# Kernel tuning notes

Measured on AMD Instinct MI355X. Metric: run time of the kernel, lower is better.

Reference implementation:

```python
import jax, jax.numpy as jnp
import numpy as np

B, T = 128, 51            # batch, token sequence length (cond token prepended -> T+1=52)
C, H = 1024, 16           # embed_dim, n_head
L = 8                     # total Blocks: 4 in trans_base + 4 in trans_head
F = 4 * C                 # fc_rate * embed_dim
V = 1024                  # num_vq
CLIP = 512
EPS = 1e-5


def sincos_pe(seq_len, dim):
    # faithful to pos_encoding.PE1d_sincos
    pos = np.arange(seq_len, dtype=np.float32)[:, None]
    div = np.exp(np.arange(0, dim, 2, dtype=np.float32) * (-np.log(10000.0) / dim))
    pe = np.zeros((seq_len, dim), np.float32)
    pe[:, 0::2] = np.sin(pos * div)
    pe[:, 1::2] = np.cos(pos * div)
    return jnp.asarray(pe)


def setup_inputs() -> dict:
    key = jax.random.key(0)
    ks = jax.random.split(key, 12)
    s = 0.02  # init std per _init_weights
    nrm = lambda k, shape: jax.random.normal(k, shape, jnp.float32) * s
    return dict(
        idx=jax.random.randint(ks[0], (B, T), 0, V + 2),
        clip_feature=jax.random.normal(ks[1], (B, CLIP), jnp.float32),
        tok_emb=nrm(ks[2], (V + 2, C)),
        cond_w=nrm(ks[3], (CLIP, C)), cond_b=jnp.zeros((C,), jnp.float32),
        ln1_w=jnp.ones((L, C), jnp.float32), ln1_b=jnp.zeros((L, C), jnp.float32),
        wq=nrm(ks[4], (L, C, C)), bq=jnp.zeros((L, C), jnp.float32),
        wk=nrm(ks[5], (L, C, C)), bk=jnp.zeros((L, C), jnp.float32),
        wv=nrm(ks[6], (L, C, C)), bv=jnp.zeros((L, C), jnp.float32),
        wp=nrm(ks[7], (L, C, C)), bp=jnp.zeros((L, C), jnp.float32),
        ln2_w=jnp.ones((L, C), jnp.float32), ln2_b=jnp.zeros((L, C), jnp.float32),
        w1=nrm(ks[8], (L, C, F)), b1=jnp.zeros((L, F), jnp.float32),
        w2=nrm(ks[9], (L, F, C)), b2=jnp.zeros((L, C), jnp.float32),
        lnf_w=jnp.ones((C,), jnp.float32), lnf_b=jnp.zeros((C,), jnp.float32),
        head_w=nrm(ks[10], (C, V + 1)),
    )


def _ln(x, w, b):
    m = jnp.mean(x, axis=-1, keepdims=True)
    v = jnp.var(x, axis=-1, keepdims=True)
    return (x - m) * jax.lax.rsqrt(v + EPS) * w + b


def _block(x, ln1w, ln1b, wq, bq, wk, bk, wv, bv, wp, bp, ln2w, ln2b, w1, b1, w2, b2):
    b_, t_, c_ = x.shape
    d = c_ // H
    h = _ln(x, ln1w, ln1b)
    q = (h @ wq + bq).reshape(b_, t_, H, d).transpose(0, 2, 1, 3)  # [B,H,T,d]
    k = (h @ wk + bk).reshape(b_, t_, H, d).transpose(0, 2, 1, 3)
    v = (h @ wv + bv).reshape(b_, t_, H, d).transpose(0, 2, 1, 3)
    att = jnp.einsum('bhqd,bhkd->bhqk', q, k) * (1.0 / np.sqrt(d))
    causal = jnp.tril(jnp.ones((t_, t_), bool))
    att = jnp.where(causal, att, -jnp.inf)
    att = jax.nn.softmax(att, axis=-1)
    y = jnp.einsum('bhqk,bhkd->bhqd', att, v).transpose(0, 2, 1, 3).reshape(b_, t_, c_)
    x = x + y @ wp + bp
    h2 = _ln(x, ln2w, ln2b)
    x = x + jax.nn.gelu(h2 @ w1 + b1, approximate=False) @ w2 + b2
    return x


def reference(idx, clip_feature, tok_emb, cond_w, cond_b,
              ln1_w, ln1_b, wq, bq, wk, bk, wv, bv, wp, bp,
              ln2_w, ln2_b, w1, b1, w2, b2, lnf_w, lnf_b, head_w):
    # CrossCondTransBase: cond token + token embeddings + sinusoidal pos embed
    cond = (clip_feature @ cond_w + cond_b)[:, None, :]           # [B,1,C]
    tok = tok_emb[idx]                                            # [B,T,C]
    x = jnp.concatenate([cond, tok], axis=1)                      # [B,T+1,C]
    x = x + sincos_pe(x.shape[1], C)[None, :, :]
    # 4 base blocks + 4 head blocks (identical structure, stacked params)
    for i in range(L):
        x = _block(x, ln1_w[i], ln1_b[i], wq[i], bq[i], wk[i], bk[i],
                   wv[i], bv[i], wp[i], bp[i], ln2_w[i], ln2_b[i],
                   w1[i], b1[i], w2[i], b2[i])
    x = _ln(x, lnf_w, lnf_b)
    logits = x @ head_w                                           # [B,T+1,num_vq+1]
    return logits
```

## Files before the change

### kernel.cpp

```cpp
#include <hip/hip_runtime.h>

using bf16x8 = __attribute__((ext_vector_type(8))) __bf16;
using short8 = __attribute__((ext_vector_type(8))) short;
using u16x8  = __attribute__((ext_vector_type(8))) unsigned short;
using u16x4  = __attribute__((ext_vector_type(4))) unsigned short;
using f32x4  = __attribute__((ext_vector_type(4))) float;

#define DEVI __device__ __forceinline__

DEVI unsigned short f2bf(float f) {
  union { float f; unsigned u; } un; un.f = f;
  unsigned r = un.u + 0x7fffu + ((un.u >> 16) & 1u);
  return (unsigned short)(r >> 16);
}

typedef const __attribute__((address_space(1))) void* gas1_t;
typedef __attribute__((address_space(3))) void* las3_t;

DEVI void gload16(const void* g, void* lds) {
  __builtin_amdgcn_global_load_lds(
      reinterpret_cast<gas1_t>(reinterpret_cast<unsigned long long>(g)),
      reinterpret_cast<las3_t>(static_cast<unsigned>(reinterpret_cast<unsigned long long>(lds))),
      16, 0, 0);
}

#define VMW(n) asm volatile("s_waitcnt vmcnt(" #n ")" ::: "memory")
#define LGK0   do { asm volatile("s_waitcnt lgkmcnt(0)" ::: "memory"); __builtin_amdgcn_sched_barrier(0); } while (0)
#define BARS   do { __builtin_amdgcn_s_barrier(); __builtin_amdgcn_sched_barrier(0); } while (0)

__global__ void __launch_bounds__(256)
transpose_cvt(const float* __restrict__ src, unsigned short* __restrict__ dst,
              int K, int N, int Nrows, long srcStride, long dstStride) {
  src += (size_t)blockIdx.z * srcStride;
  dst += (size_t)blockIdx.z * dstStride;
  __shared__ float tile[32][33];
  const int n0 = blockIdx.x * 32, k0 = blockIdx.y * 32;
  const int tx = threadIdx.x & 31, ty = threadIdx.x >> 5;
#pragma unroll
  for (int i = 0; i < 4; ++i) {
    const int kk = ty + i * 8;
    const int n = n0 + tx;
    tile[kk][tx] = (n < N) ? src[(size_t)(k0 + kk) * N + n] : 0.f;
  }
  __syncthreads();
#pragma unroll
  for (int i = 0; i < 4; ++i) {
    const int nn = ty + i * 8;
    const int n = n0 + nn;
    if (n < Nrows) dst[(size_t)n * K + k0 + tx] = f2bf(tile[tx][nn]);
  }
}

__global__ void __launch_bounds__(256)
concat_bias(const float* __restrict__ bq, const float* __restrict__ bk,
            const float* __restrict__ bv, float* __restrict__ ob) {
  const int i = blockIdx.x * 256 + threadIdx.x;
  if (i >= 8 * 3072) return;
  const int l = i / 3072, c = i - l * 3072;
  float v;
  if (c < 1024)      v = bq[l * 1024 + c];
  else if (c < 2048) v = bk[l * 1024 + c - 1024];
  else               v = bv[l * 1024 + c - 2048];
  ob[i] = v;
}

__global__ void __launch_bounds__(256)
embed_kernel(const int* __restrict__ idx, const float* __restrict__ clip,
             const float* __restrict__ tok_emb, const float* __restrict__ cond_w,
             const float* __restrict__ cond_b, float* __restrict__ x) {
  const int row = blockIdx.x;
  const int b = row / 52, t = row - b * 52;
  const int c0 = threadIdx.x * 4;
  float e[4];
  if (t == 0) {
    e[0] = cond_b[c0]; e[1] = cond_b[c0 + 1]; e[2] = cond_b[c0 + 2]; e[3] = cond_b[c0 + 3];
    for (int k = 0; k < 512; ++k) {
      const float cf = clip[b * 512 + k];
      const float4 wv = *(const float4*)&cond_w[k * 1024 + c0];
      e[0] += cf * wv.x; e[1] += cf * wv.y; e[2] += cf * wv.z; e[3] += cf * wv.w;
    }
  } else {
    const int tok = idx[b * 51 + t - 1];
    const float4 tv = *(const float4*)&tok_emb[(size_t)tok * 1024 + c0];
    e[0] = tv.x; e[1] = tv.y; e[2] = tv.z; e[3] = tv.w;
  }
  const float nl = -9.2103403719761836f / 1024.0f;
#pragma unroll
  for (int j = 0; j < 4; ++j) {
    const int c = c0 + j;
    const float dv = expf((float)(c & ~1) * nl);
    const float ang = (float)t * dv;
    e[j] += (c & 1) ? cosf(ang) : sinf(ang);
  }
  float4 o; o.x = e[0]; o.y = e[1]; o.z = e[2]; o.w = e[3];
  *(float4*)&x[(size_t)row * 1024 + c0] = o;
}

__global__ void __launch_bounds__(256)
ln_kernel(const float* __restrict__ x, const float* __restrict__ w,
          const float* __restrict__ bsh, unsigned short* __restrict__ out) {
  const size_t row = blockIdx.x;
  const int tid = threadIdx.x;
  const float4 v = *(const float4*)&x[row * 1024 + tid * 4];
  float s1 = v.x + v.y + v.z + v.w;
  float s2 = v.x * v.x + v.y * v.y + v.z * v.z + v.w * v.w;
#pragma unroll
  for (int m = 1; m < 64; m <<= 1) { s1 += __shfl_xor(s1, m); s2 += __shfl_xor(s2, m); }
  __shared__ float red[8];
  const int wid = tid >> 6;
  if ((tid & 63) == 0) { red[wid] = s1; red[4 + wid] = s2; }
  __syncthreads();
  s1 = red[0] + red[1] + red[2] + red[3];
  s2 = red[4] + red[5] + red[6] + red[7];
  const float mean = s1 * (1.0f / 1024.0f);
  const float var  = s2 * (1.0f / 1024.0f) - mean * mean;
  const float rstd = rsqrtf(var + 1e-5f);
  const float4 wv = *(const float4*)&w[tid * 4];
  const float4 bv = *(const float4*)&bsh[tid * 4];
  ushort4 o;
  o.x = f2bf((v.x - mean) * rstd * wv.x + bv.x);
  o.y = f2bf((v.y - mean) * rstd * wv.y + bv.y);
  o.z = f2bf((v.z - mean) * rstd * wv.z + bv.z);
  o.w = f2bf((v.w - mean) * rstd * wv.w + bv.w);
  *(ushort4*)&out[row * 1024 + tid * 4] = o;
}

__global__ void __launch_bounds__(256)
ln_sum_kernel(const float* __restrict__ xold, const float* __restrict__ part,
              long pstride, int S, const float* __restrict__ fcb,
              const float* __restrict__ w, const float* __restrict__ bsh,
              float* __restrict__ xnew, unsigned short* __restrict__ hout) {
  const size_t row = blockIdx.x;
  const int tid = threadIdx.x;
  const float4 xv = *(const float4*)&xold[row * 1024 + tid * 4];
  const float4 bb = *(const float4*)&fcb[tid * 4];
  float e0 = xv.x + bb.x, e1 = xv.y + bb.y, e2 = xv.z + bb.z, e3 = xv.w + bb.w;
  for (int s = 0; s < S; ++s) {
    const float4 p = *(const float4*)&part[(size_t)s * pstride + row * 1024 + tid * 4];
    e0 += p.x; e1 += p.y; e2 += p.z; e3 += p.w;
  }
  float s1 = e0 + e1 + e2 + e3;
  float s2 = e0 * e0 + e1 * e1 + e2 * e2 + e3 * e3;
#pragma unroll
  for (int m = 1; m < 64; m <<= 1) { s1 += __shfl_xor(s1, m); s2 += __shfl_xor(s2, m); }
  __shared__ float red[8];
  const int wid = tid >> 6;
  if ((tid & 63) == 0) { red[wid] = s1; red[4 + wid] = s2; }
  __syncthreads();
  s1 = red[0] + red[1] + red[2] + red[3];
  s2 = red[4] + red[5] + red[6] + red[7];
  const float mean = s1 * (1.0f / 1024.0f);
  const float var  = s2 * (1.0f / 1024.0f) - mean * mean;
  const float rstd = rsqrtf(var + 1e-5f);
  float4 xo; xo.x = e0; xo.y = e1; xo.z = e2; xo.w = e3;
  *(float4*)&xnew[row * 1024 + tid * 4] = xo;
  const float4 wv = *(const float4*)&w[tid * 4];
  const float4 bv = *(const float4*)&bsh[tid * 4];
  ushort4 o;
  o.x = f2bf((e0 - mean) * rstd * wv.x + bv.x);
  o.y = f2bf((e1 - mean) * rstd * wv.y + bv.y);
  o.z = f2bf((e2 - mean) * rstd * wv.z + bv.z);
  o.w = f2bf((e3 - mean) * rstd * wv.w + bv.w);
  *(ushort4*)&hout[row * 1024 + tid * 4] = o;
}

template <int EPI>
__global__ void __launch_bounds__(512, 2)
gemm256(const unsigned short* __restrict__ A, const unsigned short* __restrict__ WT,
        const float* __restrict__ bias, void* outp,
        int Kfull, int N, int k_len, int ny, int nz) {
  constexpr bool SWAP = (EPI == 0 || EPI == 1);
  __shared__ unsigned short smem[49152];
  const int tid = threadIdx.x;
  const int lane = tid & 63;
  const int wid = tid >> 6;
  const int lrow = lane & 15, lkg = lane >> 4;
  const int wm = wid >> 2, wn = wid & 3;

  const int nwg = gridDim.x;
  int bid = blockIdx.x;
  {
    const int q = nwg >> 3, r = nwg & 7;
    const int xcd = bid & 7, i = bid >> 3;
    bid = ((xcd < r) ? xcd * (q + 1) : r * (q + 1) + (xcd - r) * q) + i;
  }
  const int nxy = nwg / nz;
  const int z = bid / nxy;
  const int rem = bid - z * nxy;
  const int nx = nxy / ny;
  const int yt = rem / nx;
  const int xt = rem - yt * nx;
  const long m0 = (long)xt * 256;
  const long n0 = (long)yt * 256;
  const int kb = z * k_len;

  const unsigned short* ag[2];
  const unsigned short* bg[2];
#pragma unroll
  for (int j = 0; j < 2; ++j) {
    const int c = tid + j * 512;
    const int f = c >> 6, kg = (c >> 4) & 3, r = c & 15;
    ag[j] = A  + (m0 + f * 16 + r) * (long)Kfull + kb + kg * 8;
    bg[j] = WT + (n0 + f * 16 + r) * (long)Kfull + kb + kg * 8;
  }
  const int lo0 = wid * 512;
  const int lo1 = 4096 + wid * 512;

  f32x4 acc[8][4] = {};
  const int T = k_len >> 5;

  auto STAGE = [&](int t) {
    const int bo = (t % 3) * 16384;
    const long kt = (long)t * 32;
    gload16(ag[0] + kt, smem + bo + lo0);
    gload16(ag[1] + kt, smem + bo + lo1);
    gload16(bg[0] + kt, smem + bo + 8192 + lo0);
    gload16(bg[1] + kt, smem + bo + 8192 + lo1);
  };

  STAGE(0); STAGE(1);

  for (int t = 0; t < T; ++t) {
    if (t + 1 < T) VMW(4);
    else           VMW(0);
    BARS;
    if (t + 2 < T) STAGE(t + 2);
    const int bo = (t % 3) * 16384;
    bf16x8 afr[8], bfr[4];
#pragma unroll
    for (int m = 0; m < 8; ++m) afr[m] = *(const bf16x8*)&smem[bo + (wm * 8 + m) * 512 + lane * 8];
#pragma unroll
    for (int n = 0; n < 4; ++n) bfr[n] = *(const bf16x8*)&smem[bo + 8192 + (wn * 4 + n) * 512 + lane * 8];
    LGK0;
    __builtin_amdgcn_s_setprio(1);
#pragma unroll
    for (int m = 0; m < 8; ++m)
#pragma unroll
      for (int n = 0; n < 4; ++n) {
        if constexpr (SWAP)
          acc[m][n] = __builtin_amdgcn_mfma_f32_16x16x32_bf16(bfr[n], afr[m], acc[m][n], 0, 0, 0);
        else
          acc[m][n] = __builtin_amdgcn_mfma_f32_16x16x32_bf16(afr[m], bfr[n], acc[m][n], 0, 0, 0);
      }
    __builtin_amdgcn_s_setprio(0);
  }

  if constexpr (SWAP) {
#pragma unroll
    for (int p = 0; p < 2; ++p) {
      __syncthreads();
      if (wm == p) {
#pragma unroll
        for (int m = 0; m < 8; ++m) {
          const int rowl = m * 16 + lrow;
          const unsigned rb = (unsigned)rowl * 512;
          const unsigned sw = (unsigned)(rowl & 7) << 4;
#pragma unroll
          for (int n = 0; n < 4; ++n) {
            const int colb = wn * 64 + n * 16 + lkg * 4;
            const float4 bv = *(const float4*)&bias[n0 + colb];
            float v0 = acc[m][n][0] + bv.x;
            float v1 = acc[m][n][1] + bv.y;
            float v2 = acc[m][n][2] + bv.z;
            float v3 = acc[m][n][3] + bv.w;
            if constexpr (EPI == 1) {
              v0 = 0.5f * v0 * (1.0f + erff(v0 * 0.70710678118654752f));
              v1 = 0.5f * v1 * (1.0f + erff(v1 * 0.70710678118654752f));
              v2 = 0.5f * v2 * (1.0f + erff(v2 * 0.70710678118654752f));
              v3 = 0.5f * v3 * (1.0f + erff(v3 * 0.70710678118654752f));
            }
            u16x4 o = { f2bf(v0), f2bf(v1), f2bf(v2), f2bf(v3) };
            *(u16x4*)((char*)smem + ((rb + colb * 2) ^ sw)) = o;
          }
        }
      }
      __syncthreads();
      unsigned short* out = (unsigned short*)outp;
#pragma unroll
      for (int i = 0; i < 8; ++i) {
        const int idx = tid + i * 512;
        const int rowl = idx >> 5, c32 = idx & 31;
        const unsigned byteoff = ((unsigned)rowl * 512 + (unsigned)c32 * 16) ^ ((unsigned)(rowl & 7) << 4);
        const u16x8 v = *(const u16x8*)((const char*)smem + byteoff);
        *(u16x8*)&out[(m0 + p * 128 + rowl) * (long)N + n0 + c32 * 8] = v;
      }
    }
  } else {
    float* out = (float*)outp + (size_t)z * ((size_t)(nxy / ny) * 256) * N;
#pragma unroll
    for (int n = 0; n < 4; ++n) {
      const int col = (int)n0 + wn * 64 + n * 16 + lrow;
#pragma unroll
      for (int m = 0; m < 8; ++m) {
        const long rowb = m0 + wm * 128 + m * 16 + lkg * 4;
#pragma unroll
        for (int r = 0; r < 4; ++r)
          out[(rowb + r) * (long)N + col] = acc[m][n][r];
      }
    }
  }
}

template <int EPI>
__global__ void __launch_bounds__(256)
gemm128(const unsigned short* __restrict__ A, const unsigned short* __restrict__ WT,
        const float* __restrict__ bias, const float* res, void* outp,
        int Kfull, int N, int k_len, int ny, int nz) {
  __shared__ unsigned short smem[24576];
  const int tid = threadIdx.x;
  const int lane = tid & 63;
  const int wid = tid >> 6;
  const int lrow = lane & 15, lkg = lane >> 4;
  const int wr = wid >> 1, wc = wid & 1;

  const int nwg = gridDim.x;
  int bid = blockIdx.x;
  {
    const int q = nwg >> 3, r = nwg & 7;
    const int xcd = bid & 7, i = bid >> 3;
    bid = ((xcd < r) ? xcd * (q + 1) : r * (q + 1) + (xcd - r) * q) + i;
  }
  const int nxy = nwg / nz;
  const int z = bid / nxy;
  const int rem = bid - z * nxy;
  const int nx = nxy / ny;
  const int yt = rem / nx;
  const int xt = rem - yt * nx;
  const long m0 = (long)xt * 128;
  const long n0 = (long)yt * 128;
  const int kb = z * k_len;

  const unsigned short* a0 = A + (m0 + (wid * 2 + 0) * 16 + lrow) * (long)Kfull + kb + lkg * 8;
  const unsigned short* a1 = A + (m0 + (wid * 2 + 1) * 16 + lrow) * (long)Kfull + kb + lkg * 8;
  const unsigned short* b0 = WT + (n0 + (wid * 2 + 0) * 16 + lrow) * (long)Kfull + kb + lkg * 8;
  const unsigned short* b1 = WT + (n0 + (wid * 2 + 1) * 16 + lrow) * (long)Kfull + kb + lkg * 8;
  const int so0 = (wid * 2 + 0) * 512, so1 = (wid * 2 + 1) * 512;

  f32x4 acc[4][4] = {};
  const int T = k_len >> 5;

  auto STAGE = [&](int t) {
    const int boff = (t % 3) * 8192;
    const int kt = t * 32;
    gload16(a0 + kt, smem + boff + so0);
    gload16(a1 + kt, smem + boff + so1);
    gload16(b0 + kt, smem + boff + 4096 + so0);
    gload16(b1 + kt, smem + boff + 4096 + so1);
  };

  STAGE(0);
  STAGE(1);

  for (int t = 0; t < T; ++t) {
    if (t + 1 < T) asm volatile("s_waitcnt vmcnt(4)" ::: "memory");
    else           asm volatile("s_waitcnt vmcnt(0)" ::: "memory");
    __builtin_amdgcn_s_barrier();
    __builtin_amdgcn_sched_barrier(0);
    if (t + 2 < T) STAGE(t + 2);
    const int cb = (t % 3) * 8192;
    bf16x8 af[4], bf8[4];
#pragma unroll
    for (int m = 0; m < 4; ++m) af[m] = *(const bf16x8*)&smem[cb + (wr * 4 + m) * 512 + lane * 8];
#pragma unroll
    for (int n = 0; n < 4; ++n) bf8[n] = *(const bf16x8*)&smem[cb + 4096 + (wc * 4 + n) * 512 + lane * 8];
#pragma unroll
    for (int m = 0; m < 4; ++m)
#pragma unroll
      for (int n = 0; n < 4; ++n)
        acc[m][n] = __builtin_amdgcn_mfma_f32_16x16x32_bf16(af[m], bf8[n], acc[m][n], 0, 0, 0);
  }
  __syncthreads();

#pragma unroll
  for (int n = 0; n < 4; ++n) {
    const int col = (int)n0 + wc * 64 + n * 16 + lrow;
    const bool cv = col < N;
    float bv = 0.f;
    if (EPI == 2) bv = cv ? bias[col] : 0.f;
#pragma unroll
    for (int m = 0; m < 4; ++m) {
      const long rowb = m0 + wr * 64 + m * 16 + lkg * 4;
#pragma unroll
      for (int r = 0; r < 4; ++r) {
        float v = acc[m][n][r] + bv;
        if (cv) {
          if constexpr (EPI == 2)
            ((float*)outp)[(rowb + r) * (long)N + col] = res[(rowb + r) * (long)N + col] + v;
          else
            ((float*)outp)[(rowb + r) * (long)N + col] = v;
        }
      }
    }
  }
}

__global__ void __launch_bounds__(256)
attn_kernel(const unsigned short* __restrict__ qkv,
            unsigned short* __restrict__ attno) {
  __shared__ unsigned short qA[4096];
  __shared__ unsigned short kB[4096];
  __shared__ unsigned short vB[4096];
  __shared__ unsigned short pA[4096];
  const int bh = blockIdx.x;
  const int b = bh >> 4, h = bh & 15;
  const int tid = threadIdx.x;
  const int lane = tid & 63;
  const int wid = tid >> 6;
  const int lrow = lane & 15, lkg = lane >> 4;

  for (int i = tid; i < 512; i += 256) {
    const int row = i >> 3;
    const int dc = i & 7;
    short8 qv = {}, kv = {}, vv = {};
    if (row < 52) {
      const unsigned short* base = qkv + ((size_t)(b * 52 + row)) * 3072 + h * 64 + dc * 8;
      qv = *(const short8*)(base);
      kv = *(const short8*)(base + 1024);
      vv = *(const short8*)(base + 2048);
    }
    *(short8*)&qA[(row >> 4) * 1024 + dc * 128 + (row & 15) * 8] = qv;
    *(short8*)&kB[(row >> 4) * 1024 + dc * 128 + (row & 15) * 8] = kv;
#pragma unroll
    for (int j = 0; j < 8; ++j) {
      const int d = dc * 8 + j;
      vB[(d >> 4) * 1024 + (row >> 3) * 128 + (d & 15) * 8 + (row & 7)] = (unsigned short)vv[j];
    }
  }
  __syncthreads();

  f32x4 sacc[4] = {};
#pragma unroll
  for (int s = 0; s < 2; ++s) {
    const bf16x8 a = *(const bf16x8*)&qA[wid * 1024 + s * 512 + lane * 8];
#pragma unroll
    for (int c = 0; c < 4; ++c) {
      const bf16x8 bb = *(const bf16x8*)&kB[c * 1024 + s * 512 + lane * 8];
      sacc[c] = __builtin_amdgcn_mfma_f32_16x16x32_bf16(a, bb, sacc[c], 0, 0, 0);
    }
  }

#pragma unroll
  for (int r = 0; r < 4; ++r) {
    const int trow = wid * 16 + lkg * 4 + r;
    float sv[4];
#pragma unroll
    for (int c = 0; c < 4; ++c) {
      const int kp = c * 16 + lrow;
      sv[c] = (kp <= trow && kp < 52) ? sacc[c][r] * 0.125f : -3.0e38f;
    }
    float mx = fmaxf(fmaxf(sv[0], sv[1]), fmaxf(sv[2], sv[3]));
#pragma unroll
    for (int m = 1; m < 16; m <<= 1) mx = fmaxf(mx, __shfl_xor(mx, m));
    float p[4], sum = 0.f;
#pragma unroll
    for (int c = 0; c < 4; ++c) { p[c] = __expf(sv[c] - mx); sum += p[c]; }
#pragma unroll
    for (int m = 1; m < 16; m <<= 1) sum += __shfl_xor(sum, m);
    const float inv = 1.0f / sum;
#pragma unroll
    for (int c = 0; c < 4; ++c) {
      const int kp = c * 16 + lrow;
      pA[wid * 1024 + (kp >> 3) * 128 + (lkg * 4 + r) * 8 + (kp & 7)] = f2bf(p[c] * inv);
    }
  }
  __syncthreads();

  f32x4 oacc[4] = {};
#pragma unroll
  for (int s = 0; s < 2; ++s) {
    const bf16x8 a = *(const bf16x8*)&pA[wid * 1024 + s * 512 + lane * 8];
#pragma unroll
    for (int db = 0; db < 4; ++db) {
      const bf16x8 bb = *(const bf16x8*)&vB[db * 1024 + s * 512 + lane * 8];
      oacc[db] = __builtin_amdgcn_mfma_f32_16x16x32_bf16(a, bb, oacc[db], 0, 0, 0);
    }
  }
#pragma unroll
  for (int db = 0; db < 4; ++db)
#pragma unroll
    for (int r = 0; r < 4; ++r) {
      const int trow = wid * 16 + lkg * 4 + r;
      if (trow < 52) {
        const int d = db * 16 + lrow;
        attno[((size_t)(b * 52 + trow)) * 1024 + h * 64 + d] = f2bf(oacc[db][r]);
      }
    }
}

extern "C" void kernel_launch(void* const* d_in, const int* in_sizes, int n_in,
                              void* d_out, int out_size, void* d_ws, size_t ws_size,
                              hipStream_t stream) {
  const int*   idx    = (const int*)d_in[0];
  const float* clip   = (const float*)d_in[1];
  const float* tok    = (const float*)d_in[2];
  const float* cond_w = (const float*)d_in[3];
  const float* cond_b = (const float*)d_in[4];
  const float* ln1w   = (const float*)d_in[5];
  const float* ln1b   = (const float*)d_in[6];
  const float* wq     = (const float*)d_in[7];
  const float* bq     = (const float*)d_in[8];
  const float* wk     = (const float*)d_in[9];
  const float* bk     = (const float*)d_in[10];
  const float* wv     = (const float*)d_in[11];
  const float* bv     = (const float*)d_in[12];
  const float* wp     = (const float*)d_in[13];
  const float* bp     = (const float*)d_in[14];
  const float* ln2w   = (const float*)d_in[15];
  const float* ln2b   = (const float*)d_in[16];
  const float* w1     = (const float*)d_in[17];
  const float* b1     = (const float*)d_in[18];
  const float* w2     = (const float*)d_in[19];
  const float* b2     = (const float*)d_in[20];
  const float* lnfw   = (const float*)d_in[21];
  const float* lnfb   = (const float*)d_in[22];
  const float* headw  = (const float*)d_in[23];

  const int M = 6656;
  char* ws = (char*)d_ws;
  size_t off = 0;
  auto alloc = [&](size_t bytes) -> void* {
    void* p = ws + off;
    off += (bytes + 255) & ~(size_t)255;
    return p;
  };

  unsigned short* qkvT  = (unsigned short*)alloc((size_t)8 * 3072 * 1024 * 2);
  unsigned short* wpT   = (unsigned short*)alloc((size_t)8 * 1024 * 1024 * 2);
  unsigned short* w1T   = (unsigned short*)alloc((size_t)8 * 4096 * 1024 * 2);
  unsigned short* w2T   = (unsigned short*)alloc((size_t)8 * 1024 * 4096 * 2);
  unsigned short* headT = (unsigned short*)alloc((size_t)1152 * 1024 * 2);
  float*          qkvB  = (float*)alloc((size_t)8 * 3072 * 4);
  float*          xbuf  = (float*)alloc((size_t)M * 1024 * 4);
  unsigned short* hbuf  = (unsigned short*)alloc((size_t)M * 1024 * 2);
  unsigned short* big   = (unsigned short*)alloc((size_t)M * 4096 * 2);
  unsigned short* attno = (unsigned short*)alloc((size_t)M * 1024 * 2);
  float*          pbuf  = (float*)alloc((size_t)2 * M * 1024 * 4);
  unsigned short* qkv  = big;
  unsigned short* mlph = big;
  const long ps1024 = (long)M * 1024;

  const dim3 tb(256);
  const dim3 tb512(512);
  transpose_cvt<<<dim3(32, 32, 8), tb, 0, stream>>>(wq, qkvT,                        1024, 1024, 1024, (long)1024 * 1024, (long)3072 * 1024);
  transpose_cvt<<<dim3(32, 32, 8), tb, 0, stream>>>(wk, qkvT + (size_t)1024 * 1024,  1024, 1024, 1024, (long)1024 * 1024, (long)3072 * 1024);
  transpose_cvt<<<dim3(32, 32, 8), tb, 0, stream>>>(wv, qkvT + (size_t)2048 * 1024,  1024, 1024, 1024, (long)1024 * 1024, (long)3072 * 1024);
  transpose_cvt<<<dim3(32, 32, 8), tb, 0, stream>>>(wp, wpT,  1024, 1024, 1024, (long)1024 * 1024, (long)1024 * 1024);
  transpose_cvt<<<dim3(128, 32, 8), tb, 0, stream>>>(w1, w1T, 1024, 4096, 4096, (long)1024 * 4096, (long)4096 * 1024);
  transpose_cvt<<<dim3(32, 128, 8), tb, 0, stream>>>(w2, w2T, 4096, 1024, 1024, (long)4096 * 1024, (long)1024 * 4096);
  transpose_cvt<<<dim3(36, 32, 1), tb, 0, stream>>>(headw, headT, 1024, 1025, 1152, 0, 0);
  concat_bias<<<dim3(96), tb, 0, stream>>>(bq, bk, bv, qkvB);
  embed_kernel<<<dim3(M), tb, 0, stream>>>(idx, clip, tok, cond_w, cond_b, xbuf);
  ln_kernel<<<dim3(M), tb, 0, stream>>>(xbuf, ln1w, ln1b, hbuf);

  for (int l = 0; l < 8; ++l) {
    gemm256<0><<<dim3(312), tb512, 0, stream>>>(hbuf, qkvT + (size_t)l * 3072 * 1024,
                                                qkvB + l * 3072, qkv, 1024, 3072, 1024, 12, 1);
    attn_kernel<<<dim3(2048), tb, 0, stream>>>(qkv, attno);
    gemm128<2><<<dim3(52 * 8), tb, 0, stream>>>(attno, wpT + (size_t)l * 1024 * 1024,
                                                bp + l * 1024, xbuf, xbuf, 1024, 1024, 1024, 8, 1);
    ln_kernel<<<dim3(M), tb, 0, stream>>>(xbuf, ln2w + l * 1024, ln2b + l * 1024, hbuf);
    gemm256<1><<<dim3(416), tb512, 0, stream>>>(hbuf, w1T + (size_t)l * 4096 * 1024,
                                                b1 + l * 4096, mlph, 1024, 4096, 1024, 16, 1);
    gemm256<4><<<dim3(208), tb512, 0, stream>>>(mlph, w2T + (size_t)l * 1024 * 4096,
                                                nullptr, pbuf, 4096, 1024, 2048, 4, 2);
    if (l < 7)
      ln_sum_kernel<<<dim3(M), tb, 0, stream>>>(xbuf, pbuf, ps1024, 2, b2 + l * 1024,
                                                ln1w + (l + 1) * 1024, ln1b + (l + 1) * 1024, xbuf, hbuf);
    else
      ln_sum_kernel<<<dim3(M), tb, 0, stream>>>(xbuf, pbuf, ps1024, 2, b2 + l * 1024,
                                                lnfw, lnfb, xbuf, hbuf);
  }
  gemm128<3><<<dim3(52 * 9), tb, 0, stream>>>(hbuf, headT, nullptr, nullptr, d_out, 1024, 1025, 1024, 9, 1);
}
```

Before: 3.305 ms.

## Switch 256-tile GEMM to double-buffered 64-wide K stages with single-pass epilogue

The 256x256 GEMM now stages 64 K-elements per step into two 64KB-total LDS buffers instead of three 32-wide buffers, issuing loads in two 32-wide halves interleaved with compute. The epilogue writes the whole 256x256 bf16 tile to LDS in one pass rather than two halves, removing two barriers. Block-to-tile mapping in both GEMM kernels is changed to iterate N tiles fastest, altering L2 reuse patterns. The larger LDS footprint (128KB) may reduce occupancy below the two blocks per CU the launch bounds request.

```diff
diff --git a/kernel.cpp b/kernel.cpp
--- a/kernel.cpp
+++ b/kernel.cpp
@@ -170,7 +170,7 @@
         const float* __restrict__ bias, void* outp,
         int Kfull, int N, int k_len, int ny, int nz) {
   constexpr bool SWAP = (EPI == 0 || EPI == 1);
-  __shared__ unsigned short smem[49152];
+  __shared__ unsigned short smem[65536];
   const int tid = threadIdx.x;
   const int lane = tid & 63;
   const int wid = tid >> 6;
@@ -187,103 +187,99 @@
   const int nxy = nwg / nz;
   const int z = bid / nxy;
   const int rem = bid - z * nxy;
-  const int nx = nxy / ny;
-  const int yt = rem / nx;
-  const int xt = rem - yt * nx;
+  const int xt = rem / ny;
+  const int yt = rem - xt * ny;
   const long m0 = (long)xt * 256;
   const long n0 = (long)yt * 256;
   const int kb = z * k_len;
 
-  const unsigned short* ag[2];
-  const unsigned short* bg[2];
+  const unsigned short* aS[2];
+  const unsigned short* bS[2];
 #pragma unroll
   for (int j = 0; j < 2; ++j) {
-    const int c = tid + j * 512;
-    const int f = c >> 6, kg = (c >> 4) & 3, r = c & 15;
-    ag[j] = A  + (m0 + f * 16 + r) * (long)Kfull + kb + kg * 8;
-    bg[j] = WT + (n0 + f * 16 + r) * (long)Kfull + kb + kg * 8;
-  }
-  const int lo0 = wid * 512;
-  const int lo1 = 4096 + wid * 512;
+    const int f = j * 8 + wid;
+    aS[j] = A  + (m0 + f * 16 + lrow) * (long)Kfull + kb + lkg * 8;
+    bS[j] = WT + (n0 + f * 16 + lrow) * (long)Kfull + kb + lkg * 8;
+  }
+
+  auto STU = [&](int t, int ks) {
+    const int bo = (t & 1) * 32768;
+    const long kt = (long)t * 64 + ks * 32;
+    gload16(aS[0] + kt, smem + bo + ks * 8192 + wid * 512);
+    gload16(aS[1] + kt, smem + bo + ks * 8192 + (8 + wid) * 512);
+    gload16(bS[0] + kt, smem + bo + 16384 + ks * 8192 + wid * 512);
+    gload16(bS[1] + kt, smem + bo + 16384 + ks * 8192 + (8 + wid) * 512);
+  };
 
   f32x4 acc[8][4] = {};
-  const int T = k_len >> 5;
-
-  auto STAGE = [&](int t) {
-    const int bo = (t % 3) * 16384;
-    const long kt = (long)t * 32;
-    gload16(ag[0] + kt, smem + bo + lo0);
-    gload16(ag[1] + kt, smem + bo + lo1);
-    gload16(bg[0] + kt, smem + bo + 8192 + lo0);
-    gload16(bg[1] + kt, smem + bo + 8192 + lo1);
-  };
-
-  STAGE(0); STAGE(1);
+  const int T = k_len >> 6;
+
+  STU(0, 0); STU(0, 1);
 
   for (int t = 0; t < T; ++t) {
-    if (t + 1 < T) VMW(4);
-    else           VMW(0);
-    BARS;
-    if (t + 2 < T) STAGE(t + 2);
-    const int bo = (t % 3) * 16384;
+    const int bo = (t & 1) * 32768;
     bf16x8 afr[8], bfr[4];
 #pragma unroll
-    for (int m = 0; m < 8; ++m) afr[m] = *(const bf16x8*)&smem[bo + (wm * 8 + m) * 512 + lane * 8];
-#pragma unroll
-    for (int n = 0; n < 4; ++n) bfr[n] = *(const bf16x8*)&smem[bo + 8192 + (wn * 4 + n) * 512 + lane * 8];
-    LGK0;
-    __builtin_amdgcn_s_setprio(1);
-#pragma unroll
-    for (int m = 0; m < 8; ++m)
+    for (int ks = 0; ks < 2; ++ks) {
+      if (t + 1 < T || ks == 0) VMW(4);
+      else                      VMW(0);
+      BARS;
+      if (t + 1 < T) STU(t + 1, ks);
+#pragma unroll
+      for (int m = 0; m < 8; ++m)
+        afr[m] = *(const bf16x8*)&smem[bo + ks * 8192 + (wm * 8 + m) * 512 + lane * 8];
+#pragma unroll
+      for (int n = 0; n < 4; ++n)
+        bfr[n] = *(const bf16x8*)&smem[bo + 16384 + ks * 8192 + (wn * 4 + n) * 512 + lane * 8];
+      LGK0;
+      __builtin_amdgcn_s_setprio(1);
+#pragma unroll
+      for (int m = 0; m < 8; ++m)
+#pragma unroll
+        for (int n = 0; n < 4; ++n) {
+          if constexpr (SWAP)
+            acc[m][n] = __builtin_amdgcn_mfma_f32_16x16x32_bf16(bfr[n], afr[m], acc[m][n], 0, 0, 0);
+          else
+            acc[m][n] = __builtin_amdgcn_mfma_f32_16x16x32_bf16(afr[m], bfr[n], acc[m][n], 0, 0, 0);
+        }
+      __builtin_amdgcn_s_setprio(0);
+    }
+  }
+  __syncthreads();
+
+  if constexpr (SWAP) {
+#pragma unroll
+    for (int m = 0; m < 8; ++m) {
+      const int row = wm * 128 + m * 16 + lrow;
+      const unsigned rb = (unsigned)row * 512;
+      const unsigned sw = (unsigned)(row & 7) << 4;
 #pragma unroll
       for (int n = 0; n < 4; ++n) {
-        if constexpr (SWAP)
-          acc[m][n] = __builtin_amdgcn_mfma_f32_16x16x32_bf16(bfr[n], afr[m], acc[m][n], 0, 0, 0);
-        else
-          acc[m][n] = __builtin_amdgcn_mfma_f32_16x16x32_bf16(afr[m], bfr[n], acc[m][n], 0, 0, 0);
+        const int colb = wn * 64 + n * 16 + lkg * 4;
+        const float4 bv = *(const float4*)&bias[n0 + colb];
+        float v0 = acc[m][n][0] + bv.x;
+        float v1 = acc[m][n][1] + bv.y;
+        float v2 = acc[m][n][2] + bv.z;
+        float v3 = acc[m][n][3] + bv.w;
+        if constexpr (EPI == 1) {
+          v0 = 0.5f * v0 * (1.0f + erff(v0 * 0.70710678118654752f));
+          v1 = 0.5f * v1 * (1.0f + erff(v1 * 0.70710678118654752f));
+          v2 = 0.5f * v2 * (1.0f + erff(v2 * 0.70710678118654752f));
+          v3 = 0.5f * v3 * (1.0f + erff(v3 * 0.70710678118654752f));
+        }
+        u16x4 o = { f2bf(v0), f2bf(v1), f2bf(v2), f2bf(v3) };
+        *(u16x4*)((char*)smem + ((rb + colb * 2) ^ sw)) = o;
       }
-    __builtin_amdgcn_s_setprio(0);
-  }
-
-  if constexpr (SWAP) {
-#pragma unroll
-    for (int p = 0; p < 2; ++p) {
-      __syncthreads();
-      if (wm == p) {
-#pragma unroll
-        for (int m = 0; m < 8; ++m) {
-          const int rowl = m * 16 + lrow;
-          const unsigned rb = (unsigned)rowl * 512;
-          const unsigned sw = (unsigned)(rowl & 7) << 4;
-#pragma unroll
-          for (int n = 0; n < 4; ++n) {
-            const int colb = wn * 64 + n * 16 + lkg * 4;
-            const float4 bv = *(const float4*)&bias[n0 + colb];
-            float v0 = acc[m][n][0] + bv.x;
-            float v1 = acc[m][n][1] + bv.y;
-            float v2 = acc[m][n][2] + bv.z;
-            float v3 = acc[m][n][3] + bv.w;
-            if constexpr (EPI == 1) {
-              v0 = 0.5f * v0 * (1.0f + erff(v0 * 0.70710678118654752f));
-              v1 = 0.5f * v1 * (1.0f + erff(v1 * 0.70710678118654752f));
-              v2 = 0.5f * v2 * (1.0f + erff(v2 * 0.70710678118654752f));
-              v3 = 0.5f * v3 * (1.0f + erff(v3 * 0.70710678118654752f));
-            }
-            u16x4 o = { f2bf(v0), f2bf(v1), f2bf(v2), f2bf(v3) };
-            *(u16x4*)((char*)smem + ((rb + colb * 2) ^ sw)) = o;
-          }
-        }
-      }
-      __syncthreads();
-      unsigned short* out = (unsigned short*)outp;
-#pragma unroll
-      for (int i = 0; i < 8; ++i) {
-        const int idx = tid + i * 512;
-        const int rowl = idx >> 5, c32 = idx & 31;
-        const unsigned byteoff = ((unsigned)rowl * 512 + (unsigned)c32 * 16) ^ ((unsigned)(rowl & 7) << 4);
-        const u16x8 v = *(const u16x8*)((const char*)smem + byteoff);
-        *(u16x8*)&out[(m0 + p * 128 + rowl) * (long)N + n0 + c32 * 8] = v;
-      }
+    }
+    __syncthreads();
+    unsigned short* out = (unsigned short*)outp;
+#pragma unroll
+    for (int i = 0; i < 16; ++i) {
+      const int idx = tid + i * 512;
+      const int row = idx >> 5, c32 = idx & 31;
+      const unsigned byteoff = ((unsigned)row * 512 + (unsigned)c32 * 16) ^ ((unsigned)(row & 7) << 4);
+      const u16x8 v = *(const u16x8*)((const char*)smem + byteoff);
+      *(u16x8*)&out[(m0 + row) * (long)N + n0 + c32 * 8] = v;
     }
   } else {
     float* out = (float*)outp + (size_t)z * ((size_t)(nxy / ny) * 256) * N;
@@ -323,9 +319,8 @@
   const int nxy = nwg / nz;
   const int z = bid / nxy;
   const int rem = bid - z * nxy;
-  const int nx = nxy / ny;
-  const int yt = rem / nx;
-  const int xt = rem - yt * nx;
+  const int xt = rem / ny;
+  const int yt = rem - xt * ny;
   const long m0 = (long)xt * 128;
   const long n0 = (long)yt * 128;
   const int kb = z * k_len;
```

Result: faster. 3.012 ms (-8.9%).
